# Optimization experiments

Hardware: AMD Instinct MI355X
Metric: run time of the kernel (lower is better)

## Reference

```python
import jax, jax.numpy as jnp
import numpy as np

D_MODEL = 2048
N_HEADS = 16
HEAD_DIM = D_MODEL // N_HEADS
ROPE_THETA = 10000.0
B, S = 2, 2048
MAX_POS = 8192


def _rope(x, position_ids):
    # x: [b, h, s, hd]; position_ids: [b, s] int
    half = HEAD_DIM // 2
    inv_freq = 1.0 / (ROPE_THETA ** (jnp.arange(0, HEAD_DIM, 2, dtype=jnp.float32) / HEAD_DIM))  # [half]
    ang = position_ids[..., None].astype(jnp.float32) * inv_freq  # [b, s, half]
    cos = jnp.concatenate([jnp.cos(ang), jnp.cos(ang)], axis=-1)[:, None]  # [b, 1, s, hd]
    sin = jnp.concatenate([jnp.sin(ang), jnp.sin(ang)], axis=-1)[:, None]
    x1, x2 = x[..., :half], x[..., half:]
    rot = jnp.concatenate([-x2, x1], axis=-1)  # rotate_half
    return x * cos + rot * sin


def setup_inputs() -> dict:
    key = jax.random.key(0)
    ks = jax.random.split(key, 6)
    wscale = 1.0 / np.sqrt(D_MODEL)
    x_sparse = jax.random.normal(ks[0], (B, S, D_MODEL), dtype=jnp.float32)
    Wq = jax.random.normal(ks[1], (D_MODEL, D_MODEL), dtype=jnp.float32) * wscale
    Wk = jax.random.normal(ks[2], (D_MODEL, D_MODEL), dtype=jnp.float32) * wscale
    Wv = jax.random.normal(ks[3], (D_MODEL, D_MODEL), dtype=jnp.float32) * wscale
    Wo = jax.random.normal(ks[4], (D_MODEL, D_MODEL), dtype=jnp.float32) * wscale
    position_ids = jnp.sort(jax.random.randint(ks[5], (B, S), 0, MAX_POS), axis=-1).astype(jnp.int64)
    return {"x_sparse": x_sparse, "Wq": Wq, "Wk": Wk, "Wv": Wv, "Wo": Wo, "position_ids": position_ids}


def reference(x_sparse, Wq, Wk, Wv, Wo, position_ids):
    b, s, d = x_sparse.shape

    def heads(W):
        return (x_sparse @ W).reshape(b, s, N_HEADS, HEAD_DIM).transpose(0, 2, 1, 3)  # [b,h,s,hd]

    q = _rope(heads(Wq), position_ids)
    k = _rope(heads(Wk), position_ids)
    v = heads(Wv)

    scores = jnp.einsum('bhqd,bhkd->bhqk', q, k) / np.float32(np.sqrt(HEAD_DIM))
    # dynamic position-based causal mask: pos_i >= pos_j, broadcast over heads
    mask = position_ids[:, None, :, None] >= position_ids[:, None, None, :]  # [b,1,s,s]
    scores = jnp.where(mask, scores, jnp.float32(-1e30))
    attn = jax.nn.softmax(scores, axis=-1)
    out = jnp.einsum('bhqk,bhkd->bhqd', attn, v)  # [b,h,s,hd]
    out = out.transpose(0, 2, 1, 3).reshape(b, s, d)
    return out @ Wo
```

## Files before the change

### kernel.cpp

```cpp
#include <hip/hip_runtime.h>
#include <stdint.h>


typedef unsigned short u16;
typedef unsigned int u32;
typedef __attribute__((ext_vector_type(8))) short bf16x8;
typedef __attribute__((ext_vector_type(4))) float f32x4;

#define SEQ 2048
#define DM 2048
#define NH 16
#define HD 128
#define SM_SCALE 0.08838834764831845f

__device__ __forceinline__ u16 f2bf(float f) {
  union { float f; uint32_t u; } v; v.f = f;
  uint32_t u = v.u + 0x7fffu + ((v.u >> 16) & 1u);
  return (u16)(u >> 16);
}
__device__ __forceinline__ float bf2f(u16 h) {
  union { uint32_t u; float f; } v; v.u = ((uint32_t)h) << 16; return v.f;
}
__device__ __forceinline__ u32 pack2(float a, float b) {
  return (u32)f2bf(a) | ((u32)f2bf(b) << 16);
}

__device__ __forceinline__ void gl2lds16(const void* g, void* l) {
  __builtin_amdgcn_global_load_lds(
      (const __attribute__((address_space(1))) uint32_t*)g,
      (__attribute__((address_space(3))) uint32_t*)l, 16, 0, 0);
}

__global__ __launch_bounds__(256) void cvt_x(const float* __restrict__ x, u16* __restrict__ xb) {
  int i = blockIdx.x * 256 + threadIdx.x;
  float4 v = ((const float4*)x)[i];
  uint2 r;
  r.x = pack2(v.x, v.y);
  r.y = pack2(v.z, v.w);
  ((uint2*)xb)[i] = r;
}

__global__ __launch_bounds__(256) void wtrans(const float* __restrict__ w0, const float* __restrict__ w1,
                                              const float* __restrict__ w2, const float* __restrict__ w3,
                                              u16* __restrict__ dst) {
  const float* W = blockIdx.z == 0 ? w0 : blockIdx.z == 1 ? w1 : blockIdx.z == 2 ? w2 : w3;
  u16* D = dst + (size_t)blockIdx.z * DM * DM;
  int k0 = blockIdx.x * 32, n0 = blockIdx.y * 32;
  __shared__ u16 t[32][33];
  int tx = threadIdx.x, ty = threadIdx.y;
#pragma unroll
  for (int i = 0; i < 32; i += 8)
    t[ty + i][tx] = f2bf(W[(size_t)(k0 + ty + i) * DM + n0 + tx]);
  __syncthreads();
#pragma unroll
  for (int i = 0; i < 32; i += 8)
    D[(size_t)(n0 + ty + i) * DM + k0 + tx] = t[tx][ty + i];
}

__device__ __forceinline__ void gemm_core(const u16* __restrict__ A, const u16* __restrict__ Bt,
                                          int m0, int n0, u16* As, u16* Bs, f32x4 acc[4][4]) {
  int tid = threadIdx.x, lane = tid & 63;
  int l15 = lane & 15, quad = lane >> 4;
  int wave = tid >> 6;
  int wm = (wave >> 1) * 64, wn = (wave & 1) * 64;
  for (int k0 = 0; k0 < DM; k0 += 64) {
#pragma unroll
    for (int i = 0; i < 4; ++i) {
      int s = i * 256 + tid;
      int row = s >> 3, c = (s & 7) ^ (row & 7);
      gl2lds16(&A[(size_t)(m0 + row) * DM + k0 + c * 8], &As[(s & ~63) * 8]);
      gl2lds16(&Bt[(size_t)(n0 + row) * DM + k0 + c * 8], &Bs[(s & ~63) * 8]);
    }
    __syncthreads();
#pragma unroll
    for (int kk = 0; kk < 2; ++kk) {
      bf16x8 af[4], bfr[4];
#pragma unroll
      for (int mt = 0; mt < 4; ++mt) {
        int row = wm + mt * 16 + l15;
        int c = (kk * 4 + quad) ^ (row & 7);
        af[mt] = *(const bf16x8*)&As[row * 64 + c * 8];
      }
#pragma unroll
      for (int nt = 0; nt < 4; ++nt) {
        int row = wn + nt * 16 + l15;
        int c = (kk * 4 + quad) ^ (row & 7);
        bfr[nt] = *(const bf16x8*)&Bs[row * 64 + c * 8];
      }
#pragma unroll
      for (int mt = 0; mt < 4; ++mt)
#pragma unroll
        for (int nt = 0; nt < 4; ++nt)
          acc[mt][nt] = __builtin_amdgcn_mfma_f32_16x16x32_bf16(af[mt], bfr[nt], acc[mt][nt], 0, 0, 0);
    }
    __syncthreads();
  }
}

__global__ __launch_bounds__(256) void qkv_gemm(const u16* __restrict__ X, const u16* __restrict__ Wt,
                                                u16* __restrict__ Qo, u16* __restrict__ Ko,
                                                u16* __restrict__ Vto) {
  __shared__ u16 As[128 * 64];
  __shared__ u16 Bs[128 * 64];
  const u16* Bt = Wt + (size_t)blockIdx.z * DM * DM;
  int n0 = blockIdx.x * 128, m0 = blockIdx.y * 128;
  f32x4 acc[4][4] = {};
  gemm_core(X, Bt, m0, n0, As, Bs, acc);
  int lane = threadIdx.x & 63, wave = threadIdx.x >> 6;
  int l15 = lane & 15, quad = lane >> 4;
  int wm = (wave >> 1) * 64, wn = (wave & 1) * 64;
  if (blockIdx.z == 2) {
    int h = n0 >> 7;
#pragma unroll
    for (int mt = 0; mt < 4; ++mt)
#pragma unroll
      for (int nt = 0; nt < 4; ++nt) {
        int tok = m0 + wm + mt * 16 + quad * 4;
        int d = wn + nt * 16 + l15;
        int b = tok >> 11, sx = tok & (SEQ - 1);
        u16* dp = &Vto[((size_t)(b * NH + h) * HD + d) * SEQ + sx];
        *(u32*)&dp[0] = pack2(acc[mt][nt][0], acc[mt][nt][1]);
        *(u32*)&dp[2] = pack2(acc[mt][nt][2], acc[mt][nt][3]);
      }
  } else {
    u16* C = blockIdx.z == 0 ? Qo : Ko;
#pragma unroll
    for (int mt = 0; mt < 4; ++mt)
#pragma unroll
      for (int nt = 0; nt < 4; ++nt)
#pragma unroll
        for (int r = 0; r < 4; ++r)
          C[(size_t)(m0 + wm + mt * 16 + quad * 4 + r) * DM + n0 + wn + nt * 16 + l15]
              = f2bf(acc[mt][nt][r]);
  }
}

__global__ __launch_bounds__(256) void proj_gemm(const u16* __restrict__ A, const u16* __restrict__ Wt,
                                                 float* __restrict__ C) {
  __shared__ u16 As[128 * 64];
  __shared__ u16 Bs[128 * 64];
  int n0 = blockIdx.x * 128, m0 = blockIdx.y * 128;
  f32x4 acc[4][4] = {};
  gemm_core(A, Wt, m0, n0, As, Bs, acc);
  int lane = threadIdx.x & 63, wave = threadIdx.x >> 6;
  int l15 = lane & 15, quad = lane >> 4;
  int wm = (wave >> 1) * 64, wn = (wave & 1) * 64;
#pragma unroll
  for (int mt = 0; mt < 4; ++mt)
#pragma unroll
    for (int nt = 0; nt < 4; ++nt)
#pragma unroll
      for (int r = 0; r < 4; ++r)
        C[(size_t)(m0 + wm + mt * 16 + quad * 4 + r) * DM + n0 + wn + nt * 16 + l15] = acc[mt][nt][r];
}

__global__ __launch_bounds__(256) void rope_k(u16* __restrict__ Q, u16* __restrict__ K,
                                              const int* __restrict__ pos) {
  uint32_t idx = blockIdx.x * 256 + threadIdx.x;
  int i = idx & 63;
  int h = (idx >> 6) & 15;
  int s = (idx >> 10) & 2047;
  int b = idx >> 21;
  u16* P = (blockIdx.y == 0) ? Q : K;
  int p = pos[b * SEQ + s];
  float inv = exp2f((float)i * -0.20762051f);
  float ang = (float)p * inv;
  float sn, cs;
  sincosf(ang, &sn, &cs);
  size_t base = ((size_t)(b * SEQ + s)) * DM + h * HD;
  float x1 = bf2f(P[base + i]), x2 = bf2f(P[base + 64 + i]);
  P[base + i] = f2bf(x1 * cs - x2 * sn);
  P[base + 64 + i] = f2bf(x2 * cs + x1 * sn);
}

__global__ __launch_bounds__(256) void attn_k(const u16* __restrict__ Q, const u16* __restrict__ K,
                                              const u16* __restrict__ Vt, const int* __restrict__ pos,
                                              u16* __restrict__ AO) {
  __shared__ u16 Ks[2][64 * 128];
  __shared__ u16 Vs[2][128 * 64];
  __shared__ int pk[2][64];
  int qt = (int)gridDim.x - 1 - (int)blockIdx.x;
  int bh = blockIdx.y;
  int b = bh >> 4, h = bh & 15;
  int tid = threadIdx.x, lane = tid & 63, wave = tid >> 6;
  int l15 = lane & 15, quad = lane >> 4;
  const int* posb = pos + b * SEQ;
  int q0w = qt * 64 + wave * 16;
  const u16* Kbase = &K[(size_t)(b * SEQ) * DM + h * HD];
  const u16* Vbase = &Vt[(size_t)(b * NH + h) * HD * SEQ];

  bf16x8 qf[4];
#pragma unroll
  for (int kk = 0; kk < 4; ++kk)
    qf[kk] = *(const bf16x8*)&Q[(size_t)(b * SEQ + q0w + l15) * DM + h * HD + kk * 32 + quad * 8];
  int pq = posb[q0w + l15];
  int pqmax = posb[qt * 64 + 63];

  int ntile = 1;
  while (ntile < 32 && posb[ntile * 64] <= pqmax) ++ntile;

  {
    int j0 = 0;
#pragma unroll
    for (int i = 0; i < 4; ++i) {
      int s = i * 256 + tid;
      { int row = s >> 4, c = (s & 15) ^ (row & 15);
        gl2lds16(&Kbase[(size_t)(j0 + row) * DM + c * 8], &Ks[0][(s & ~63) * 8]); }
      { int row = s >> 3, c = (s & 7) ^ (row & 7);
        gl2lds16(&Vbase[(size_t)row * SEQ + j0 + c * 8], &Vs[0][(s & ~63) * 8]); }
    }
    if (tid < 64) pk[0][tid] = posb[j0 + tid];
  }

  float m_i = -1.0e30f, l_i = 0.0f;
  f32x4 oacc[8] = {};

  for (int j = 0; j < ntile; ++j) {
    int cur = j & 1;
    __syncthreads();

    if (j + 1 < ntile) {
      int j0n = (j + 1) * 64, alt = cur ^ 1;
#pragma unroll
      for (int i = 0; i < 4; ++i) {
        int s = i * 256 + tid;
        { int row = s >> 4, c = (s & 15) ^ (row & 15);
          gl2lds16(&Kbase[(size_t)(j0n + row) * DM + c * 8], &Ks[alt][(s & ~63) * 8]); }
        { int row = s >> 3, c = (s & 7) ^ (row & 7);
          gl2lds16(&Vbase[(size_t)row * SEQ + j0n + c * 8], &Vs[alt][(s & ~63) * 8]); }
      }
      if (tid < 64) pk[alt][tid] = posb[j0n + tid];
    }

    f32x4 sacc[4] = {};
#pragma unroll
    for (int kk = 0; kk < 4; ++kk) {
      bf16x8 kf[4];
#pragma unroll
      for (int kt = 0; kt < 4; ++kt) {
        int row = kt * 16 + l15;
        int c = (kk * 4 + quad) ^ (row & 15);
        kf[kt] = *(const bf16x8*)&Ks[cur][row * 128 + c * 8];
      }
#pragma unroll
      for (int kt = 0; kt < 4; ++kt)
        sacc[kt] = __builtin_amdgcn_mfma_f32_16x16x32_bf16(kf[kt], qf[kk], sacc[kt], 0, 0, 0);
    }

    int4 pkv[4];
#pragma unroll
    for (int kt = 0; kt < 4; ++kt) pkv[kt] = *(const int4*)&pk[cur][kt * 16 + quad * 4];
    float mx = -3.0e38f;
#pragma unroll
    for (int kt = 0; kt < 4; ++kt) {
      const int* pr = (const int*)&pkv[kt];
#pragma unroll
      for (int r = 0; r < 4; ++r) {
        float s = sacc[kt][r] * SM_SCALE;
        s = (pq >= pr[r]) ? s : -1.0e30f;
        sacc[kt][r] = s;
        mx = fmaxf(mx, s);
      }
    }
    mx = fmaxf(mx, __shfl_xor(mx, 16));
    mx = fmaxf(mx, __shfl_xor(mx, 32));
    float mn = fmaxf(m_i, mx);
    float al = __expf(m_i - mn);
    m_i = mn;
    float rs = 0.0f;
    u32 pb[4][2];
#pragma unroll
    for (int kt = 0; kt < 4; ++kt) {
      float p0 = __expf(sacc[kt][0] - mn), p1 = __expf(sacc[kt][1] - mn);
      float p2 = __expf(sacc[kt][2] - mn), p3 = __expf(sacc[kt][3] - mn);
      rs += (p0 + p1) + (p2 + p3);
      pb[kt][0] = pack2(p0, p1);
      pb[kt][1] = pack2(p2, p3);
    }
    rs += __shfl_xor(rs, 16);
    rs += __shfl_xor(rs, 32);
    l_i = l_i * al + rs;
#pragma unroll
    for (int dt = 0; dt < 8; ++dt) oacc[dt] *= al;

    int base0 = l15 + ((quad & 1) << 5);
    bool hi = (quad >> 1) != 0;
#pragma unroll
    for (int kk = 0; kk < 2; ++kk) {
      u32 w[4];
#pragma unroll
      for (int wd = 0; wd < 4; ++wd) {
        int src = base0 + ((wd >> 1) << 4);
        u32 va = __shfl(pb[kk * 2 + 0][wd & 1], src);
        u32 vb = __shfl(pb[kk * 2 + 1][wd & 1], src);
        w[wd] = hi ? vb : va;
      }
      union { bf16x8 v; u32 u[4]; } pt;
      pt.u[0] = w[0]; pt.u[1] = w[1]; pt.u[2] = w[2]; pt.u[3] = w[3];
#pragma unroll
      for (int dt = 0; dt < 8; ++dt) {
        int row = dt * 16 + l15;
        int c = (kk * 4 + quad) ^ (row & 7);
        bf16x8 vf = *(const bf16x8*)&Vs[cur][row * 64 + c * 8];
        oacc[dt] = __builtin_amdgcn_mfma_f32_16x16x32_bf16(vf, pt.v, oacc[dt], 0, 0, 0);
      }
    }
  }

  float inv = 1.0f / l_i;
  u16* aop = &AO[(size_t)(b * SEQ + q0w + l15) * DM + h * HD];
#pragma unroll
  for (int dt = 0; dt < 8; ++dt) {
    int col = dt * 16 + quad * 4;
    *(u32*)&aop[col]     = pack2(oacc[dt][0] * inv, oacc[dt][1] * inv);
    *(u32*)&aop[col + 2] = pack2(oacc[dt][2] * inv, oacc[dt][3] * inv);
  }
}

extern "C" void kernel_launch(void* const* d_in, const int* in_sizes, int n_in,
                              void* d_out, int out_size, void* d_ws, size_t ws_size,
                              hipStream_t stream) {
  const float* x  = (const float*)d_in[0];
  const float* Wq = (const float*)d_in[1];
  const float* Wk = (const float*)d_in[2];
  const float* Wv = (const float*)d_in[3];
  const float* Wo = (const float*)d_in[4];
  const int*  pos = (const int*)d_in[5];
  float* out = (float*)d_out;

  u16* ws  = (u16*)d_ws;
  u16* xb  = ws;
  u16* wt  = xb  + (size_t)4096 * 2048;
  u16* qb  = wt  + (size_t)4 * 2048 * 2048;
  u16* kb  = qb  + (size_t)4096 * 2048;
  u16* vtb = kb  + (size_t)4096 * 2048;
  u16* aob = vtb + (size_t)4096 * 2048;

  cvt_x<<<8192, 256, 0, stream>>>(x, xb);
  wtrans<<<dim3(64, 64, 4), dim3(32, 8), 0, stream>>>(Wq, Wk, Wv, Wo, wt);
  qkv_gemm<<<dim3(16, 32, 3), 256, 0, stream>>>(xb, wt, qb, kb, vtb);
  rope_k<<<dim3(16384, 2), 256, 0, stream>>>(qb, kb, pos);
  attn_k<<<dim3(32, 32), 256, 0, stream>>>(qb, kb, vtb, pos, aob);
  proj_gemm<<<dim3(16, 32), 256, 0, stream>>>(aob, wt + (size_t)3 * 2048 * 2048, out);
}
```

Baseline: 475.9 us.

## Process 128 queries per attention block to reuse K/V tiles across two sub-tiles

Each attention block now handles two 64-query sub-tiles (each wave owns two 16-row groups), so every K/V tile loaded into LDS feeds twice the MFMA work, and the grid is halved. Each V fragment is read from LDS once and used for both sub-tiles. Query-tile order is reversed for batch 1 only, which interleaves heavy and light causal blocks. The cost is more registers per thread (two sets of accumulators and Q fragments), which may lower occupancy, and fewer blocks (512), which gives coarser load balance under the causal mask.

Result: no change. 469.5 us (-1.3%).

```diff
diff --git a/kernel.cpp b/kernel.cpp
--- a/kernel.cpp
+++ b/kernel.cpp
@@ -179,41 +179,43 @@
   __shared__ u16 Ks[2][64 * 128];
   __shared__ u16 Vs[2][128 * 64];
   __shared__ int pk[2][64];
-  int qt = (int)gridDim.x - 1 - (int)blockIdx.x;
-  int bh = blockIdx.y;
+  int bx = blockIdx.x, bh = blockIdx.y;
   int b = bh >> 4, h = bh & 15;
+  int qt = b ? (15 - bx) : bx;
   int tid = threadIdx.x, lane = tid & 63, wave = tid >> 6;
   int l15 = lane & 15, quad = lane >> 4;
   const int* posb = pos + b * SEQ;
-  int q0w = qt * 64 + wave * 16;
+  int qbase = qt * 128 + wave * 16;
   const u16* Kbase = &K[(size_t)(b * SEQ) * DM + h * HD];
   const u16* Vbase = &Vt[(size_t)(b * NH + h) * HD * SEQ];
 
-  bf16x8 qf[4];
-#pragma unroll
-  for (int kk = 0; kk < 4; ++kk)
-    qf[kk] = *(const bf16x8*)&Q[(size_t)(b * SEQ + q0w + l15) * DM + h * HD + kk * 32 + quad * 8];
-  int pq = posb[q0w + l15];
-  int pqmax = posb[qt * 64 + 63];
+  bf16x8 qf[2][4];
+  int pq[2];
+#pragma unroll
+  for (int qi = 0; qi < 2; ++qi) {
+#pragma unroll
+    for (int kk = 0; kk < 4; ++kk)
+      qf[qi][kk] = *(const bf16x8*)&Q[(size_t)(b * SEQ + qbase + qi * 64 + l15) * DM
+                                      + h * HD + kk * 32 + quad * 8];
+    pq[qi] = posb[qbase + qi * 64 + l15];
+  }
+  int pqmax = posb[qt * 128 + 127];
 
   int ntile = 1;
   while (ntile < 32 && posb[ntile * 64] <= pqmax) ++ntile;
 
-  {
-    int j0 = 0;
-#pragma unroll
-    for (int i = 0; i < 4; ++i) {
-      int s = i * 256 + tid;
-      { int row = s >> 4, c = (s & 15) ^ (row & 15);
-        gl2lds16(&Kbase[(size_t)(j0 + row) * DM + c * 8], &Ks[0][(s & ~63) * 8]); }
-      { int row = s >> 3, c = (s & 7) ^ (row & 7);
-        gl2lds16(&Vbase[(size_t)row * SEQ + j0 + c * 8], &Vs[0][(s & ~63) * 8]); }
-    }
-    if (tid < 64) pk[0][tid] = posb[j0 + tid];
-  }
-
-  float m_i = -1.0e30f, l_i = 0.0f;
-  f32x4 oacc[8] = {};
+#pragma unroll
+  for (int i = 0; i < 4; ++i) {
+    int s = i * 256 + tid;
+    { int row = s >> 4, c = (s & 15) ^ (row & 15);
+      gl2lds16(&Kbase[(size_t)row * DM + c * 8], &Ks[0][(s & ~63) * 8]); }
+    { int row = s >> 3, c = (s & 7) ^ (row & 7);
+      gl2lds16(&Vbase[(size_t)row * SEQ + c * 8], &Vs[0][(s & ~63) * 8]); }
+  }
+  if (tid < 64) pk[0][tid] = posb[tid];
+
+  float m_i[2] = {-1.0e30f, -1.0e30f}, l_i[2] = {0.0f, 0.0f};
+  f32x4 oacc[2][8] = {};
 
   for (int j = 0; j < ntile; ++j) {
     int cur = j & 1;
@@ -232,7 +234,7 @@
       if (tid < 64) pk[alt][tid] = posb[j0n + tid];
     }
 
-    f32x4 sacc[4] = {};
+    f32x4 sacc[2][4] = {};
 #pragma unroll
     for (int kk = 0; kk < 4; ++kk) {
       bf16x8 kf[4];
@@ -243,77 +245,93 @@
         kf[kt] = *(const bf16x8*)&Ks[cur][row * 128 + c * 8];
       }
 #pragma unroll
-      for (int kt = 0; kt < 4; ++kt)
-        sacc[kt] = __builtin_amdgcn_mfma_f32_16x16x32_bf16(kf[kt], qf[kk], sacc[kt], 0, 0, 0);
+      for (int qi = 0; qi < 2; ++qi)
+#pragma unroll
+        for (int kt = 0; kt < 4; ++kt)
+          sacc[qi][kt] = __builtin_amdgcn_mfma_f32_16x16x32_bf16(kf[kt], qf[qi][kk], sacc[qi][kt], 0, 0, 0);
     }
 
     int4 pkv[4];
 #pragma unroll
     for (int kt = 0; kt < 4; ++kt) pkv[kt] = *(const int4*)&pk[cur][kt * 16 + quad * 4];
-    float mx = -3.0e38f;
-#pragma unroll
-    for (int kt = 0; kt < 4; ++kt) {
-      const int* pr = (const int*)&pkv[kt];
-#pragma unroll
-      for (int r = 0; r < 4; ++r) {
-        float s = sacc[kt][r] * SM_SCALE;
-        s = (pq >= pr[r]) ? s : -1.0e30f;
-        sacc[kt][r] = s;
-        mx = fmaxf(mx, s);
-      }
-    }
-    mx = fmaxf(mx, __shfl_xor(mx, 16));
-    mx = fmaxf(mx, __shfl_xor(mx, 32));
-    float mn = fmaxf(m_i, mx);
-    float al = __expf(m_i - mn);
-    m_i = mn;
-    float rs = 0.0f;
-    u32 pb[4][2];
-#pragma unroll
-    for (int kt = 0; kt < 4; ++kt) {
-      float p0 = __expf(sacc[kt][0] - mn), p1 = __expf(sacc[kt][1] - mn);
-      float p2 = __expf(sacc[kt][2] - mn), p3 = __expf(sacc[kt][3] - mn);
-      rs += (p0 + p1) + (p2 + p3);
-      pb[kt][0] = pack2(p0, p1);
-      pb[kt][1] = pack2(p2, p3);
-    }
-    rs += __shfl_xor(rs, 16);
-    rs += __shfl_xor(rs, 32);
-    l_i = l_i * al + rs;
-#pragma unroll
-    for (int dt = 0; dt < 8; ++dt) oacc[dt] *= al;
+
+    u32 pb[2][4][2];
+    float al[2];
+#pragma unroll
+    for (int qi = 0; qi < 2; ++qi) {
+      float mx = -3.0e38f;
+#pragma unroll
+      for (int kt = 0; kt < 4; ++kt) {
+        const int* pr = (const int*)&pkv[kt];
+#pragma unroll
+        for (int r = 0; r < 4; ++r) {
+          float s = sacc[qi][kt][r] * SM_SCALE;
+          s = (pq[qi] >= pr[r]) ? s : -1.0e30f;
+          sacc[qi][kt][r] = s;
+          mx = fmaxf(mx, s);
+        }
+      }
+      mx = fmaxf(mx, __shfl_xor(mx, 16));
+      mx = fmaxf(mx, __shfl_xor(mx, 32));
+      float mn = fmaxf(m_i[qi], mx);
+      al[qi] = __expf(m_i[qi] - mn);
+      m_i[qi] = mn;
+      float rs = 0.0f;
+#pragma unroll
+      for (int kt = 0; kt < 4; ++kt) {
+        float p0 = __expf(sacc[qi][kt][0] - mn), p1 = __expf(sacc[qi][kt][1] - mn);
+        float p2 = __expf(sacc[qi][kt][2] - mn), p3 = __expf(sacc[qi][kt][3] - mn);
+        rs += (p0 + p1) + (p2 + p3);
+        pb[qi][kt][0] = pack2(p0, p1);
+        pb[qi][kt][1] = pack2(p2, p3);
+      }
+      rs += __shfl_xor(rs, 16);
+      rs += __shfl_xor(rs, 32);
+      l_i[qi] = l_i[qi] * al[qi] + rs;
+#pragma unroll
+      for (int dt = 0; dt < 8; ++dt) oacc[qi][dt] *= al[qi];
+    }
 
     int base0 = l15 + ((quad & 1) << 5);
     bool hi = (quad >> 1) != 0;
 #pragma unroll
     for (int kk = 0; kk < 2; ++kk) {
-      u32 w[4];
-#pragma unroll
-      for (int wd = 0; wd < 4; ++wd) {
-        int src = base0 + ((wd >> 1) << 4);
-        u32 va = __shfl(pb[kk * 2 + 0][wd & 1], src);
-        u32 vb = __shfl(pb[kk * 2 + 1][wd & 1], src);
-        w[wd] = hi ? vb : va;
-      }
-      union { bf16x8 v; u32 u[4]; } pt;
-      pt.u[0] = w[0]; pt.u[1] = w[1]; pt.u[2] = w[2]; pt.u[3] = w[3];
+      bf16x8 vf[8];
 #pragma unroll
       for (int dt = 0; dt < 8; ++dt) {
         int row = dt * 16 + l15;
         int c = (kk * 4 + quad) ^ (row & 7);
-        bf16x8 vf = *(const bf16x8*)&Vs[cur][row * 64 + c * 8];
-        oacc[dt] = __builtin_amdgcn_mfma_f32_16x16x32_bf16(vf, pt.v, oacc[dt], 0, 0, 0);
-      }
-    }
-  }
-
-  float inv = 1.0f / l_i;
-  u16* aop = &AO[(size_t)(b * SEQ + q0w + l15) * DM + h * HD];
-#pragma unroll
-  for (int dt = 0; dt < 8; ++dt) {
-    int col = dt * 16 + quad * 4;
-    *(u32*)&aop[col]     = pack2(oacc[dt][0] * inv, oacc[dt][1] * inv);
-    *(u32*)&aop[col + 2] = pack2(oacc[dt][2] * inv, oacc[dt][3] * inv);
+        vf[dt] = *(const bf16x8*)&Vs[cur][row * 64 + c * 8];
+      }
+#pragma unroll
+      for (int qi = 0; qi < 2; ++qi) {
+        u32 w[4];
+#pragma unroll
+        for (int wd = 0; wd < 4; ++wd) {
+          int src = base0 + ((wd >> 1) << 4);
+          u32 va = __shfl(pb[qi][kk * 2 + 0][wd & 1], src);
+          u32 vb = __shfl(pb[qi][kk * 2 + 1][wd & 1], src);
+          w[wd] = hi ? vb : va;
+        }
+        union { bf16x8 v; u32 u[4]; } pt;
+        pt.u[0] = w[0]; pt.u[1] = w[1]; pt.u[2] = w[2]; pt.u[3] = w[3];
+#pragma unroll
+        for (int dt = 0; dt < 8; ++dt)
+          oacc[qi][dt] = __builtin_amdgcn_mfma_f32_16x16x32_bf16(vf[dt], pt.v, oacc[qi][dt], 0, 0, 0);
+      }
+    }
+  }
+
+#pragma unroll
+  for (int qi = 0; qi < 2; ++qi) {
+    float inv = 1.0f / l_i[qi];
+    u16* aop = &AO[(size_t)(b * SEQ + qbase + qi * 64 + l15) * DM + h * HD];
+#pragma unroll
+    for (int dt = 0; dt < 8; ++dt) {
+      int col = dt * 16 + quad * 4;
+      *(u32*)&aop[col]     = pack2(oacc[qi][dt][0] * inv, oacc[qi][dt][1] * inv);
+      *(u32*)&aop[col + 2] = pack2(oacc[qi][dt][2] * inv, oacc[qi][dt][3] * inv);
+    }
   }
 }
 
@@ -340,6 +358,6 @@
   wtrans<<<dim3(64, 64, 4), dim3(32, 8), 0, stream>>>(Wq, Wk, Wv, Wo, wt);
   qkv_gemm<<<dim3(16, 32, 3), 256, 0, stream>>>(xb, wt, qb, kb, vtb);
   rope_k<<<dim3(16384, 2), 256, 0, stream>>>(qb, kb, pos);
-  attn_k<<<dim3(32, 32), 256, 0, stream>>>(qb, kb, vtb, pos, aob);
+  attn_k<<<dim3(16, 32), 256, 0, stream>>>(qb, kb, vtb, pos, aob);
   proj_gemm<<<dim3(16, 32), 256, 0, stream>>>(aob, wt + (size_t)3 * 2048 * 2048, out);
 }
```
